# Performance work log

Hardware: AMD Instinct MI355X
Metric: run time of the kernel (lower is better)

Reference implementation:

```python
import jax, jax.numpy as jnp
import numpy as np

LOAD_BALANCE_WEIGHT = 0.05


def setup_inputs() -> dict:
    key = jax.random.key(0)
    ks = jax.random.split(key, 8)
    B, H, C, E = 8192, 4096, 1000, 4
    s_h = 1.0 / np.sqrt(H)
    return {
        "x": jax.random.normal(ks[0], (B, H), dtype=jnp.float32),
        "Wr": jax.random.normal(ks[1], (H, E), dtype=jnp.float32) * s_h,
        "br": jnp.zeros((E,), dtype=jnp.float32),
        "W1": jax.random.normal(ks[2], (E, H, H), dtype=jnp.float32) * s_h,
        "b1": jnp.zeros((E, H), dtype=jnp.float32),
        "W2": jax.random.normal(ks[3], (E, H, C), dtype=jnp.float32) * s_h,
        "b2": jnp.zeros((E, C), dtype=jnp.float32),
    }


def reference(x, Wr, br, W1, b1, W2, b2):
    # Router: linear gate -> softmax probs (eval mode: no noise)
    E = Wr.shape[1]
    router_logits = x @ Wr + br                     # [B, E]
    routing_weights = jax.nn.softmax(router_logits, axis=-1)
    # Hard top-1 dispatch
    idx = jnp.argmax(routing_weights, axis=-1)      # [B]
    onehot = jax.nn.one_hot(idx, E, dtype=x.dtype)  # [B, E]
    # Switch-style load-balance loss: E * sum(fraction_e * mean_prob_e)
    frac = onehot.mean(axis=0)                      # [E]
    mean_p = routing_weights.mean(axis=0)           # [E]
    load_balance_loss = LOAD_BALANCE_WEIGHT * E * jnp.sum(frac * mean_p)
    # Dense all-expert compute, then hard-select per token (same math as
    # gather/scatter dispatch in the torch loop, fully vectorized)
    h = jax.nn.gelu(jnp.einsum('bh,ehk->ebk', x, W1) + b1[:, None, :])  # [E,B,H]
    expert_out = jnp.einsum('ebk,ekc->ebc', h, W2) + b2[:, None, :]     # [E,B,C]
    logits = jnp.einsum('be,ebc->bc', onehot, expert_out)               # [B,C]
    return logits, load_balance_loss, routing_weights
```

## Files before the change

### kernel.cpp

```cpp
#include <hip/hip_runtime.h>
#include <hip/hip_bf16.h>

#define NB 8192
#define NH 4096
#define NC 1000
#define NE 4
#define NCP 1024

typedef __attribute__((ext_vector_type(4))) float f32x4;
typedef __attribute__((ext_vector_type(8))) short s16x8;
typedef __attribute__((ext_vector_type(4))) unsigned int u32x4;

__device__ __forceinline__ unsigned cvtpk(float a, float b){
  unsigned r; asm("v_cvt_pk_bf16_f32 %0, %1, %2" : "=v"(r) : "v"(a), "v"(b)); return r;
}
__device__ __forceinline__ int swz_off(int r, int s){
  return (r << 6) + (((s ^ (r ^ (r >> 2))) & 3) << 4);
}

__device__ __forceinline__ void gload16(const void* g, void* l) {
  __builtin_amdgcn_global_load_lds(
      (const __attribute__((address_space(1))) unsigned int*)g,
      (__attribute__((address_space(3))) unsigned int*)l, 16, 0, 0);
}

__device__ __forceinline__ void transpose_body(
    const float* __restrict__ ine, __hip_bfloat16* __restrict__ oute,
    int R, int C, int r0, int c0, int t)
{
  int c = c0 + (t << 2);
  unsigned o[4][16];
  if (c < C) {
    #pragma unroll
    for (int rp = 0; rp < 16; rp++) {
      f32x4 v0 = *(const f32x4*)(ine + (size_t)(r0 + 2*rp)     * C + c);
      f32x4 v1 = *(const f32x4*)(ine + (size_t)(r0 + 2*rp + 1) * C + c);
      #pragma unroll
      for (int j = 0; j < 4; j++) o[j][rp] = cvtpk(v0[j], v1[j]);
    }
  } else {
    #pragma unroll
    for (int j = 0; j < 4; j++)
      #pragma unroll
      for (int rp = 0; rp < 16; rp++) o[j][rp] = 0;
  }
  #pragma unroll
  for (int j = 0; j < 4; j++) {
    u32x4* dst = (u32x4*)(oute + (size_t)(c + j) * R + r0);
    dst[0] = (u32x4){ o[j][0],  o[j][1],  o[j][2],  o[j][3]  };
    dst[1] = (u32x4){ o[j][4],  o[j][5],  o[j][6],  o[j][7]  };
    dst[2] = (u32x4){ o[j][8],  o[j][9],  o[j][10], o[j][11] };
    dst[3] = (u32x4){ o[j][12], o[j][13], o[j][14], o[j][15] };
  }
}

__global__ __launch_bounds__(256) void prep_k(
    const float* __restrict__ x, const float* __restrict__ Wr,
    const float* __restrict__ br, float* __restrict__ out,
    int* __restrict__ idx, int* __restrict__ cnt_part, float* __restrict__ sum_part,
    __hip_bfloat16* __restrict__ xb,
    const float* __restrict__ W1, __hip_bfloat16* __restrict__ W1t,
    const float* __restrict__ W2, __hip_bfloat16* __restrict__ W2t)
{
  int blk = blockIdx.x, t = threadIdx.x;
  if (blk < 2048) {
    int e = blk >> 9, by = (blk >> 2) & 127, bx = blk & 3;
    transpose_body(W1 + (size_t)e * NH * NH, W1t + (size_t)e * NH * NH,
                   NH, NH, by << 5, bx << 10, t);
    return;
  }
  if (blk < 2560) {
    int bb = blk - 2048;
    int e = bb >> 7, by = bb & 127;
    transpose_body(W2 + (size_t)e * NH * NC, W2t + (size_t)e * NCP * NH,
                   NH, NC, by << 5, 0, t);
    return;
  }
  int b = blk - 2560;
  const float* xr = x + (size_t)b * NH;
  int h0 = t << 4;
  f32x4 v[4];
  #pragma unroll
  for (int j = 0; j < 4; j++) v[j] = *(const f32x4*)(xr + h0 + (j << 2));
  u32x4 ob0 = { cvtpk(v[0][0],v[0][1]), cvtpk(v[0][2],v[0][3]),
                cvtpk(v[1][0],v[1][1]), cvtpk(v[1][2],v[1][3]) };
  u32x4 ob1 = { cvtpk(v[2][0],v[2][1]), cvtpk(v[2][2],v[2][3]),
                cvtpk(v[3][0],v[3][1]), cvtpk(v[3][2],v[3][3]) };
  *(u32x4*)(xb + (size_t)b * NH + h0) = ob0;
  *(u32x4*)(xb + (size_t)b * NH + h0 + 8) = ob1;

  double a0=0, a1=0, a2=0, a3=0;
  #pragma unroll
  for (int i = 0; i < 16; i++) {
    float xv = v[i >> 2][i & 3];
    f32x4 w = *(const f32x4*)(Wr + (size_t)(h0 + i) * 4);
    double xd = (double)xv;
    a0 += xd * (double)w[0]; a1 += xd * (double)w[1];
    a2 += xd * (double)w[2]; a3 += xd * (double)w[3];
  }
  for (int off = 32; off; off >>= 1) {
    a0 += __shfl_down(a0, off); a1 += __shfl_down(a1, off);
    a2 += __shfl_down(a2, off); a3 += __shfl_down(a3, off);
  }
  __shared__ double red[4][4];
  int wid = t >> 6;
  if ((t & 63) == 0) { red[wid][0]=a0; red[wid][1]=a1; red[wid][2]=a2; red[wid][3]=a3; }
  __syncthreads();
  if (t == 0) {
    double l[4];
    for (int e = 0; e < 4; e++)
      l[e] = red[0][e] + red[1][e] + red[2][e] + red[3][e] + (double)br[e];
    int am = 0; double mx = l[0];
    for (int e = 1; e < 4; e++) if (l[e] > mx) { mx = l[e]; am = e; }
    double p[4], s = 0;
    for (int e = 0; e < 4; e++) { p[e] = exp(l[e] - mx); s += p[e]; }
    float* rw = out + (size_t)NB * NC + 1 + (size_t)b * 4;
    int bin = (b & 63) * 4;
    for (int e = 0; e < 4; e++) {
      float pe = (float)(p[e] / s);
      rw[e] = pe;
      atomicAdd(&sum_part[bin + e], pe);
    }
    idx[b] = am;
    atomicAdd(&cnt_part[bin + am], 1);
  }
}

__global__ __launch_bounds__(256) void router_k(
    const float* __restrict__ x, const float* __restrict__ Wr,
    const float* __restrict__ br, float* __restrict__ out,
    int* __restrict__ idx, int* __restrict__ cnt_part, float* __restrict__ sum_part)
{
  int b = blockIdx.x, t = threadIdx.x;
  const float* xr = x + (size_t)b * NH;
  double a0=0, a1=0, a2=0, a3=0;
  for (int i = 0; i < 16; i++) {
    int h = t + (i << 8);
    float xv = xr[h];
    f32x4 w = *(const f32x4*)(Wr + (size_t)h * 4);
    double xd = (double)xv;
    a0 += xd * (double)w[0]; a1 += xd * (double)w[1];
    a2 += xd * (double)w[2]; a3 += xd * (double)w[3];
  }
  for (int off = 32; off; off >>= 1) {
    a0 += __shfl_down(a0, off); a1 += __shfl_down(a1, off);
    a2 += __shfl_down(a2, off); a3 += __shfl_down(a3, off);
  }
  __shared__ double red[4][4];
  int wid = t >> 6;
  if ((t & 63) == 0) { red[wid][0]=a0; red[wid][1]=a1; red[wid][2]=a2; red[wid][3]=a3; }
  __syncthreads();
  if (t == 0) {
    double l[4];
    for (int e = 0; e < 4; e++)
      l[e] = red[0][e] + red[1][e] + red[2][e] + red[3][e] + (double)br[e];
    int am = 0; double mx = l[0];
    for (int e = 1; e < 4; e++) if (l[e] > mx) { mx = l[e]; am = e; }
    double p[4], s = 0;
    for (int e = 0; e < 4; e++) { p[e] = exp(l[e] - mx); s += p[e]; }
    float* rw = out + (size_t)NB * NC + 1 + (size_t)b * 4;
    int bin = (b & 63) * 4;
    for (int e = 0; e < 4; e++) {
      float pe = (float)(p[e] / s);
      rw[e] = pe;
      atomicAdd(&sum_part[bin + e], pe);
    }
    idx[b] = am;
    atomicAdd(&cnt_part[bin + am], 1);
  }
}

__global__ void finalize_k(const int* __restrict__ cnt_part, const float* __restrict__ sum_part,
                           int* __restrict__ counts, int* __restrict__ offs, float* __restrict__ out)
{
  int t = threadIdx.x;
  __shared__ int cc[4]; __shared__ float ss[4];
  if (t < 4) {
    int c = 0; float s = 0;
    for (int i = 0; i < 64; i++) { c += cnt_part[i*4 + t]; s += sum_part[i*4 + t]; }
    cc[t] = c; ss[t] = s; counts[t] = c;
  }
  __syncthreads();
  if (t == 0) {
    int o = 0; float loss = 0.f;
    for (int e = 0; e < 4; e++) {
      offs[e] = o; o += cc[e];
      loss += ((float)cc[e] / (float)NB) * (ss[e] / (float)NB);
    }
    out[(size_t)NB * NC] = 0.05f * (float)NE * loss;
  }
}

__global__ __launch_bounds__(256) void scatter_k(
    const int* __restrict__ idx, const int* __restrict__ offs,
    int* __restrict__ cursors, int* __restrict__ perm)
{
  int b = blockIdx.x * 256 + threadIdx.x;
  int e = idx[b];
  int lane = threadIdx.x & 63;
  for (int e2 = 0; e2 < 4; e2++) {
    unsigned long long m = __ballot(e == e2);
    if (e == e2) {
      int nbelow = __popcll(m & ((1ULL << lane) - 1ULL));
      int base = 0;
      if (nbelow == 0) base = atomicAdd(&cursors[e2], (int)__popcll(m));
      int src = __ffsll((long long)m) - 1;
      base = __shfl(base, src);
      perm[offs[e2] + base + nbelow] = b;
    }
  }
}

__global__ __launch_bounds__(256) void transpose_k(
    const float* __restrict__ in, __hip_bfloat16* __restrict__ outp,
    int R, int C, int Cout)
{
  int e = blockIdx.z;
  transpose_body(in + (size_t)e * R * C, outp + (size_t)e * Cout * R,
                 R, C, blockIdx.y << 5, blockIdx.x << 10, threadIdx.x);
}


#define DSR(off) (*(const s16x8*)(lds + (off)))

template<int MODE>
__global__ __launch_bounds__(256, 4) void gemmsb_k(
    const __hip_bfloat16* __restrict__ Ax, const __hip_bfloat16* __restrict__ Bw,
    const float* __restrict__ bias, const int* __restrict__ perm,
    const int* __restrict__ counts, const int* __restrict__ offs,
    __hip_bfloat16* __restrict__ H1out, float* __restrict__ out)
{
  int e = blockIdx.z;
  int cnt = counts[e];
  if (cnt == 0) return;

  const int NX = (MODE == 0 ? 32 : 8);
  const int NWG = NX * 64;
  const int CPX = NWG / 8;
  int flat = blockIdx.x + NX * blockIdx.y;
  int lg = (flat & 7) * CPX + (flat >> 3);
  int by = lg & 63;
  int bx = lg >> 6;

  int m0 = by << 7;
  if (m0 >= cnt) return;
  int seg = offs[e];
  int n0 = bx << 7;
  const __hip_bfloat16* Be = Bw + (size_t)e * (size_t)(MODE == 0 ? NH : NCP) * NH;

  __shared__ __align__(16) char lds[32768];
  __shared__ int rowtok[128];

  int tid = threadIdx.x;
  if (tid < 128) {
    int rr = m0 + tid; if (rr >= cnt) rr = cnt - 1;
    rowtok[tid] = perm[seg + rr];
  }
  __syncthreads();

  int lane = tid & 63, w = tid >> 6;
  int wr = w >> 1, wc = w & 1;
  int cx = lane & 15, g = lane >> 4;
  int l8 = lane >> 3, l7 = lane & 7;

  int srcoff = (l7 ^ l8) << 3;
  const __hip_bfloat16* pA[4];
  const __hip_bfloat16* pB[4];
  #pragma unroll
  for (int i = 0; i < 4; i++) {
    int r = w * 32 + i * 8 + l8;
    if constexpr (MODE == 0) {
      pA[i] = Ax + (size_t)rowtok[r] * NH + srcoff;
    } else {
      int rr = m0 + r; if (rr >= cnt) rr = cnt - 1;
      pA[i] = Ax + (size_t)(seg + rr) * NH + srcoff;
    }
    pB[i] = Be + (size_t)(n0 + r) * NH + srcoff;
  }
  int wst = w * 4096;

  int swz0 = ((0 * 4 + g) ^ (cx & 7)) << 4;
  int swz1 = ((1 * 4 + g) ^ (cx & 7)) << 4;
  int arow = (wr * 64 + cx) * 128;
  int brow = (wc * 64 + cx) * 128;

  f32x4 acc[4][4] = {};

  const int NT = NH / 64;

  for (int t = 0; t < NT; t++) {
    gload16(pA[0] + (size_t)t*64, lds + wst);
    gload16(pA[1] + (size_t)t*64, lds + wst + 1024);
    gload16(pA[2] + (size_t)t*64, lds + wst + 2048);
    gload16(pA[3] + (size_t)t*64, lds + wst + 3072);
    gload16(pB[0] + (size_t)t*64, lds + 16384 + wst);
    gload16(pB[1] + (size_t)t*64, lds + 16384 + wst + 1024);
    gload16(pB[2] + (size_t)t*64, lds + 16384 + wst + 2048);
    gload16(pB[3] + (size_t)t*64, lds + 16384 + wst + 3072);
    __syncthreads();

    s16x8 a0_[4], b0_[4], a1_[4], b1_[4];
    #pragma unroll
    for (int mf = 0; mf < 4; mf++) a0_[mf] = DSR(arow + mf*2048 + swz0);
    #pragma unroll
    for (int nf = 0; nf < 4; nf++) b0_[nf] = DSR(16384 + brow + nf*2048 + swz0);
    #pragma unroll
    for (int mf = 0; mf < 4; mf++)
      #pragma unroll
      for (int nf = 0; nf < 4; nf++)
        acc[mf][nf] = __builtin_amdgcn_mfma_f32_16x16x32_bf16(a0_[mf], b0_[nf], acc[mf][nf], 0, 0, 0);
    #pragma unroll
    for (int mf = 0; mf < 4; mf++) a1_[mf] = DSR(arow + mf*2048 + swz1);
    #pragma unroll
    for (int nf = 0; nf < 4; nf++) b1_[nf] = DSR(16384 + brow + nf*2048 + swz1);
    #pragma unroll
    for (int mf = 0; mf < 4; mf++)
      #pragma unroll
      for (int nf = 0; nf < 4; nf++)
        acc[mf][nf] = __builtin_amdgcn_mfma_f32_16x16x32_bf16(a1_[mf], b1_[nf], acc[mf][nf], 0, 0, 0);
    __syncthreads();
  }

  #pragma unroll
  for (int nf = 0; nf < 4; nf++) {
    int n = n0 + wc * 64 + nf * 16 + cx;
    if (MODE == 0 || n < NC) {
      float bv = bias[(size_t)e * (MODE == 0 ? NH : NC) + n];
      #pragma unroll
      for (int mf = 0; mf < 4; mf++) {
        f32x4 vacc = acc[mf][nf];
        #pragma unroll
        for (int i = 0; i < 4; i++) {
          int mrow = wr * 64 + mf * 16 + g * 4 + i;
          int mseg = m0 + mrow;
          if (mseg < cnt) {
            float u = vacc[i] + bv;
            if constexpr (MODE == 0) {
              float th = tanhf(0.79788456080286535588f * (u + 0.044715f * u * u * u));
              float hv = 0.5f * u * (1.0f + th);
              H1out[(size_t)(seg + mseg) * NH + n] = __float2bfloat16(hv);
            } else {
              int tok = rowtok[mrow];
              out[(size_t)tok * NC + n] = u;
            }
          }
        }
      }
    }
  }
}

__global__ __launch_bounds__(256) void gemm1_k(
    const float* __restrict__ x, const float* __restrict__ W1,
    const float* __restrict__ b1, const int* __restrict__ perm,
    const int* __restrict__ counts, const int* __restrict__ offs,
    __hip_bfloat16* __restrict__ H1)
{
  int e = blockIdx.z;
  int cnt = counts[e];
  int m0 = blockIdx.y << 7;
  if (m0 >= cnt) return;
  int seg = offs[e];
  int n0 = blockIdx.x << 7;
  const float* W1e = W1 + (size_t)e * NH * NH;

  __shared__ __align__(16) char As[128*32*2];
  __shared__ __align__(16) char Bs[128*32*2];
  __shared__ int rowtok[128];

  int t = threadIdx.x;
  if (t < 128) {
    int rr = m0 + t; if (rr >= cnt) rr = cnt - 1;
    rowtok[t] = perm[seg + rr];
  }
  __syncthreads();

  int ar0 = t >> 2, as_ = t & 3;
  int ar1 = ar0 + 64;
  const float* asrc0 = x + (size_t)rowtok[ar0] * NH + (as_ << 3);
  const float* asrc1 = x + (size_t)rowtok[ar1] * NH + (as_ << 3);
  int aw0 = swz_off(ar0, as_), aw1 = swz_off(ar1, as_);
  int bnc = t & 31, bkp = t >> 5;
  const float* bsrc0 = W1e + (size_t)(bkp << 1) * NH + n0 + (bnc << 2);
  const float* bsrc1 = bsrc0 + (size_t)16 * NH;

  f32x4 acc[4][4] = {};

  int lane = t & 63, wid = t >> 6;
  int wm = (wid >> 1) << 6, wn = (wid & 1) << 6;
  int g = lane >> 4, cx = lane & 15;
  int aoff[4], boff[4];
  #pragma unroll
  for (int f = 0; f < 4; f++) {
    aoff[f] = swz_off(wm + (f << 4) + cx, g);
    boff[f] = swz_off(wn + (f << 4) + cx, g);
  }

  for (int kt = 0; kt < NH; kt += 32) {
    {
      f32x4 v0 = *(const f32x4*)(asrc0 + kt);
      f32x4 v1 = *(const f32x4*)(asrc0 + kt + 4);
      u32x4 wv = { cvtpk(v0[0],v0[1]), cvtpk(v0[2],v0[3]), cvtpk(v1[0],v1[1]), cvtpk(v1[2],v1[3]) };
      *(u32x4*)(As + aw0) = wv;
      f32x4 u0 = *(const f32x4*)(asrc1 + kt);
      f32x4 u1 = *(const f32x4*)(asrc1 + kt + 4);
      u32x4 w2 = { cvtpk(u0[0],u0[1]), cvtpk(u0[2],u0[3]), cvtpk(u1[0],u1[1]), cvtpk(u1[2],u1[3]) };
      *(u32x4*)(As + aw1) = w2;
    }
    {
      const float* p0 = bsrc0 + (size_t)kt * NH;
      f32x4 rr0 = *(const f32x4*)p0;
      f32x4 rr1 = *(const f32x4*)(p0 + NH);
      int kp = bkp, sl = kp >> 2, sub = (kp & 3) << 2;
      #pragma unroll
      for (int j = 0; j < 4; j++) {
        int n = (bnc << 2) + j;
        *(unsigned*)(Bs + (n << 6) + (((sl ^ (n ^ (n >> 2))) & 3) << 4) + sub) = cvtpk(rr0[j], rr1[j]);
      }
      const float* p1 = bsrc1 + (size_t)kt * NH;
      f32x4 q0 = *(const f32x4*)p1;
      f32x4 q1 = *(const f32x4*)(p1 + NH);
      kp = bkp + 8; sl = kp >> 2; sub = (kp & 3) << 2;
      #pragma unroll
      for (int j = 0; j < 4; j++) {
        int n = (bnc << 2) + j;
        *(unsigned*)(Bs + (n << 6) + (((sl ^ (n ^ (n >> 2))) & 3) << 4) + sub) = cvtpk(q0[j], q1[j]);
      }
    }
    __syncthreads();
    s16x8 af[4], bfr[4];
    #pragma unroll
    for (int f = 0; f < 4; f++) {
      af[f]  = *(const s16x8*)(As + aoff[f]);
      bfr[f] = *(const s16x8*)(Bs + boff[f]);
    }
    #pragma unroll
    for (int mf = 0; mf < 4; mf++)
      #pragma unroll
      for (int nf = 0; nf < 4; nf++)
        acc[mf][nf] = __builtin_amdgcn_mfma_f32_16x16x32_bf16(af[mf], bfr[nf], acc[mf][nf], 0, 0, 0);
    __syncthreads();
  }

  const float* b1e = b1 + (size_t)e * NH;
  #pragma unroll
  for (int nf = 0; nf < 4; nf++) {
    int n = n0 + wn + (nf << 4) + cx;
    float bv = b1e[n];
    #pragma unroll
    for (int mf = 0; mf < 4; mf++) {
      #pragma unroll
      for (int i = 0; i < 4; i++) {
        int mseg = m0 + wm + (mf << 4) + (g << 2) + i;
        if (mseg < cnt) {
          float u = acc[mf][nf][i] + bv;
          float th = tanhf(0.79788456080286535588f * (u + 0.044715f * u * u * u));
          float hv = 0.5f * u * (1.0f + th);
          H1[(size_t)(seg + mseg) * NH + n] = __float2bfloat16(hv);
        }
      }
    }
  }
}

__global__ __launch_bounds__(256) void gemm2_k(
    const __hip_bfloat16* __restrict__ H1, const float* __restrict__ W2,
    const float* __restrict__ b2, const int* __restrict__ perm,
    const int* __restrict__ counts, const int* __restrict__ offs,
    float* __restrict__ out)
{
  int e = blockIdx.z;
  int cnt = counts[e];
  int m0 = blockIdx.y << 7;
  if (m0 >= cnt) return;
  int seg = offs[e];
  int n0 = blockIdx.x << 7;
  const float* W2e = W2 + (size_t)e * NH * NC;

  __shared__ __align__(16) char As[128*32*2];
  __shared__ __align__(16) char Bs[128*32*2];
  __shared__ int rowtok[128];

  int t = threadIdx.x;
  if (t < 128) {
    int rr = m0 + t; if (rr >= cnt) rr = cnt - 1;
    rowtok[t] = perm[seg + rr];
  }
  __syncthreads();

  int ar0 = t >> 2, as_ = t & 3;
  int ar1 = ar0 + 64;
  int rA0 = m0 + ar0; if (rA0 >= cnt) rA0 = cnt - 1;
  int rA1 = m0 + ar1; if (rA1 >= cnt) rA1 = cnt - 1;
  const __hip_bfloat16* asrc0 = H1 + (size_t)(seg + rA0) * NH + (as_ << 3);
  const __hip_bfloat16* asrc1 = H1 + (size_t)(seg + rA1) * NH + (as_ << 3);
  int aw0 = swz_off(ar0, as_), aw1 = swz_off(ar1, as_);

  int bnc = t & 31, bkp = t >> 5;
  int col = n0 + (bnc << 2);
  bool bvalid = col < NC;
  const float* bsrc0 = W2e + (size_t)(bkp << 1) * NC + col;
  const float* bsrc1 = bsrc0 + (size_t)16 * NC;

  f32x4 acc[4][4] = {};

  int lane = t & 63, wid = t >> 6;
  int wm = (wid >> 1) << 6, wn = (wid & 1) << 6;
  int g = lane >> 4, cx = lane & 15;
  int aoff[4], boff[4];
  #pragma unroll
  for (int f = 0; f < 4; f++) {
    aoff[f] = swz_off(wm + (f << 4) + cx, g);
    boff[f] = swz_off(wn + (f << 4) + cx, g);
  }

  for (int kt = 0; kt < NH; kt += 32) {
    {
      *(u32x4*)(As + aw0) = *(const u32x4*)(asrc0 + kt);
      *(u32x4*)(As + aw1) = *(const u32x4*)(asrc1 + kt);
    }
    {
      f32x4 rr0 = {}, rr1 = {}, q0 = {}, q1 = {};
      if (bvalid) {
        const float* p0 = bsrc0 + (size_t)kt * NC;
        rr0 = *(const f32x4*)p0; rr1 = *(const f32x4*)(p0 + NC);
        const float* p1 = bsrc1 + (size_t)kt * NC;
        q0 = *(const f32x4*)p1; q1 = *(const f32x4*)(p1 + NC);
      }
      int kp = bkp, sl = kp >> 2, sub = (kp & 3) << 2;
      #pragma unroll
      for (int j = 0; j < 4; j++) {
        int n = (bnc << 2) + j;
        *(unsigned*)(Bs + (n << 6) + (((sl ^ (n ^ (n >> 2))) & 3) << 4) + sub) = cvtpk(rr0[j], rr1[j]);
      }
      kp = bkp + 8; sl = kp >> 2; sub = (kp & 3) << 2;
      #pragma unroll
      for (int j = 0; j < 4; j++) {
        int n = (bnc << 2) + j;
        *(unsigned*)(Bs + (n << 6) + (((sl ^ (n ^ (n >> 2))) & 3) << 4) + sub) = cvtpk(q0[j], q1[j]);
      }
    }
    __syncthreads();
    s16x8 af[4], bfr[4];
    #pragma unroll
    for (int f = 0; f < 4; f++) {
      af[f]  = *(const s16x8*)(As + aoff[f]);
      bfr[f] = *(const s16x8*)(Bs + boff[f]);
    }
    #pragma unroll
    for (int mf = 0; mf < 4; mf++)
      #pragma unroll
      for (int nf = 0; nf < 4; nf++)
        acc[mf][nf] = __builtin_amdgcn_mfma_f32_16x16x32_bf16(af[mf], bfr[nf], acc[mf][nf], 0, 0, 0);
    __syncthreads();
  }

  const float* b2e = b2 + (size_t)e * NC;
  #pragma unroll
  for (int nf = 0; nf < 4; nf++) {
    int n = n0 + wn + (nf << 4) + cx;
    if (n < NC) {
      float bv = b2e[n];
      #pragma unroll
      for (int mf = 0; mf < 4; mf++) {
        #pragma unroll
        for (int i = 0; i < 4; i++) {
          int mseg = m0 + wm + (mf << 4) + (g << 2) + i;
          if (mseg < cnt) {
            int tok = rowtok[wm + (mf << 4) + (g << 2) + i];
            out[(size_t)tok * NC + n] = acc[mf][nf][i] + bv;
          }
        }
      }
    }
  }
}

extern "C" void kernel_launch(void* const* d_in, const int* in_sizes, int n_in,
                              void* d_out, int out_size, void* d_ws, size_t ws_size,
                              hipStream_t stream) {
  const float* x  = (const float*)d_in[0];
  const float* Wr = (const float*)d_in[1];
  const float* br = (const float*)d_in[2];
  const float* W1 = (const float*)d_in[3];
  const float* b1 = (const float*)d_in[4];
  const float* W2 = (const float*)d_in[5];
  const float* b2 = (const float*)d_in[6];
  float* out = (float*)d_out;

  char* ws = (char*)d_ws;
  const size_t SZ_XB  = (size_t)NB * NH * 2;
  const size_t SZ_H1  = (size_t)NB * NH * 2;
  const size_t SZ_W1T = (size_t)NE * NH * NH * 2;
  const size_t SZ_W2T = (size_t)NE * NCP * NH * 2;
  const size_t need = SZ_XB + SZ_H1 + SZ_W1T + SZ_W2T + (size_t)NB*4*2 + 4096;

  if (ws_size >= need) {
    size_t o = 0;
    __hip_bfloat16* xb  = (__hip_bfloat16*)(ws + o); o += SZ_XB;
    __hip_bfloat16* H1  = (__hip_bfloat16*)(ws + o); o += SZ_H1;
    __hip_bfloat16* W1t = (__hip_bfloat16*)(ws + o); o += SZ_W1T;
    __hip_bfloat16* W2t = (__hip_bfloat16*)(ws + o); o += SZ_W2T;
    int* idx  = (int*)(ws + o); o += (size_t)NB * 4;
    int* perm = (int*)(ws + o); o += (size_t)NB * 4;
    char* small = ws + o;
    int*   cursors  = (int*)(small);
    int*   counts   = (int*)(small + 16);
    int*   offs     = (int*)(small + 32);
    int*   cnt_part = (int*)(small + 64);
    float* sum_part = (float*)(small + 64 + 1024);

    hipMemsetAsync(small, 0, 64 + 2048, stream);
    prep_k<<<10752, 256, 0, stream>>>(x, Wr, br, out, idx, cnt_part, sum_part, xb,
                                      W1, W1t, W2, W2t);
    finalize_k<<<1, 64, 0, stream>>>(cnt_part, sum_part, counts, offs, out);
    scatter_k<<<NB / 256, 256, 0, stream>>>(idx, offs, cursors, perm);
    gemmsb_k<0><<<dim3(32, 64, 4), 256, 0, stream>>>(xb, W1t, b1, perm, counts, offs, H1, nullptr);
    gemmsb_k<1><<<dim3(8, 64, 4), 256, 0, stream>>>(H1, W2t, b2, perm, counts, offs, nullptr, out);
  } else {
    __hip_bfloat16* H1 = (__hip_bfloat16*)ws;
    size_t o = (size_t)NB * NH * 2;
    int* idx  = (int*)(ws + o); o += (size_t)NB * 4;
    int* perm = (int*)(ws + o); o += (size_t)NB * 4;
    char* small = ws + o;
    int*   cursors  = (int*)(small);
    int*   counts   = (int*)(small + 16);
    int*   offs     = (int*)(small + 32);
    int*   cnt_part = (int*)(small + 64);
    float* sum_part = (float*)(small + 64 + 1024);

    hipMemsetAsync(small, 0, 64 + 2048, stream);
    router_k<<<NB, 256, 0, stream>>>(x, Wr, br, out, idx, cnt_part, sum_part);
    finalize_k<<<1, 64, 0, stream>>>(cnt_part, sum_part, counts, offs, out);
    scatter_k<<<NB / 256, 256, 0, stream>>>(idx, offs, cursors, perm);
    gemm1_k<<<dim3(32, 64, 4), 256, 0, stream>>>(x, W1, b1, perm, counts, offs, H1);
    gemm2_k<<<dim3(8, 64, 4), 256, 0, stream>>>(H1, W2, b2, perm, counts, offs, out);
  }
}
```

Before: 750.6 us.

## Add 256x256-tile 8-wave GEMM1 kernel with double-buffered LDS pipeline

Replaces the 128x128-tile first expert GEMM with a new 512-thread kernel computing 256x256 output tiles, using 128KB of double-buffered LDS. Global-to-LDS loads are interleaved with MFMA phases, and it uses explicit vmcnt waits, barriers and setprio. Larger tiles raise arithmetic intensity and cut redundant global traffic for W1 and the gathered activations. The cost is lower occupancy and more tail waste on partially filled expert row blocks. It also removes the XCD-aware block remapping in gemmsb_k and lowers its launch-bounds occupancy hint.

```diff
diff --git a/kernel.cpp b/kernel.cpp
--- a/kernel.cpp
+++ b/kernel.cpp
@@ -221,10 +221,155 @@
 }
 
 
+#define DSR8(off) (*(const s16x8*)(lds + (off)))
+#define VMW4 asm volatile("s_waitcnt vmcnt(4)" ::: "memory")
+#define VMW0 asm volatile("s_waitcnt vmcnt(0)" ::: "memory")
+#define NOWAIT do{}while(0)
+#define NOSTG  do{}while(0)
+
+#define STG_A(TT,H) do{ \
+  gload16(pA[H][0] + (size_t)(TT)*64, lds + ((TT)&1)*32768 + (H)*16384 + wbase); \
+  gload16(pA[H][1] + (size_t)(TT)*64, lds + ((TT)&1)*32768 + (H)*16384 + wbase + 1024); \
+}while(0)
+#define STG_B(TT,H) do{ \
+  gload16(pB[H][0] + (size_t)(TT)*64, lds + 65536 + ((TT)&1)*32768 + (H)*16384 + wbase); \
+  gload16(pB[H][1] + (size_t)(TT)*64, lds + 65536 + ((TT)&1)*32768 + (H)*16384 + wbase + 1024); \
+}while(0)
+
+#define PH8(BB, MH, NQ, STG, WT) do{ \
+  s16x8 a_[4][2], b_[2][2]; \
+  _Pragma("unroll") \
+  for (int mf = 0; mf < 4; mf++) { \
+    a_[mf][0] = DSR8((BB)*32768 + (MH)*16384 + arow + mf*2048 + swz0); \
+    a_[mf][1] = DSR8((BB)*32768 + (MH)*16384 + arow + mf*2048 + swz1); \
+  } \
+  _Pragma("unroll") \
+  for (int nf = 0; nf < 2; nf++) { \
+    b_[nf][0] = DSR8(65536 + (BB)*32768 + (NQ)*16384 + brow + nf*2048 + swz0); \
+    b_[nf][1] = DSR8(65536 + (BB)*32768 + (NQ)*16384 + brow + nf*2048 + swz1); \
+  } \
+  STG; \
+  WT; \
+  __builtin_amdgcn_s_barrier(); \
+  __builtin_amdgcn_s_setprio(1); \
+  _Pragma("unroll") \
+  for (int mf = 0; mf < 4; mf++) \
+    _Pragma("unroll") \
+    for (int nf = 0; nf < 2; nf++) { \
+      acc[(MH)*2+(NQ)][mf][nf] = __builtin_amdgcn_mfma_f32_16x16x32_bf16(a_[mf][0], b_[nf][0], acc[(MH)*2+(NQ)][mf][nf], 0, 0, 0); \
+      acc[(MH)*2+(NQ)][mf][nf] = __builtin_amdgcn_mfma_f32_16x16x32_bf16(a_[mf][1], b_[nf][1], acc[(MH)*2+(NQ)][mf][nf], 0, 0, 0); \
+    } \
+  __builtin_amdgcn_s_setprio(0); \
+  __builtin_amdgcn_s_barrier(); \
+}while(0)
+
+__global__ __launch_bounds__(512, 2) void gemm1v2_k(
+    const __hip_bfloat16* __restrict__ Ax, const __hip_bfloat16* __restrict__ Bw,
+    const float* __restrict__ bias, const int* __restrict__ perm,
+    const int* __restrict__ counts, const int* __restrict__ offs,
+    __hip_bfloat16* __restrict__ H1out)
+{
+  int e = blockIdx.z;
+  int cnt = counts[e];
+  if (cnt == 0) return;
+  int m0 = blockIdx.y << 8;
+  if (m0 >= cnt) return;
+  int seg = offs[e];
+  int n0 = blockIdx.x << 8;
+  const __hip_bfloat16* Be = Bw + (size_t)e * NH * NH;
+
+  __shared__ __align__(16) char lds[131072];
+  __shared__ int rowtok[256];
+
+  int tid = threadIdx.x;
+  if (tid < 256) {
+    int rr = m0 + tid; if (rr >= cnt) rr = cnt - 1;
+    rowtok[tid] = perm[seg + rr];
+  }
+  __syncthreads();
+
+  int lane = tid & 63, w = tid >> 6;
+  int wr = w >> 2, wc = w & 3;
+  int cx = lane & 15, g = lane >> 4;
+  int l8 = lane >> 3, l7 = lane & 7;
+
+  int srcoff = (l7 ^ l8) << 3;
+  const __hip_bfloat16* pA[2][2];
+  const __hip_bfloat16* pB[2][2];
+  #pragma unroll
+  for (int h = 0; h < 2; h++)
+    #pragma unroll
+    for (int p = 0; p < 2; p++) {
+      int r = h * 128 + w * 16 + p * 8 + l8;
+      pA[h][p] = Ax + (size_t)rowtok[r] * NH + srcoff;
+      pB[h][p] = Be + (size_t)(n0 + r) * NH + srcoff;
+    }
+  int wbase = w * 2048;
+
+  int swz0 = ((0 * 4 + g) ^ (cx & 7)) << 4;
+  int swz1 = ((1 * 4 + g) ^ (cx & 7)) << 4;
+  int arow = (wr * 64 + cx) * 128;
+  int brow = (wc * 32 + cx) * 128;
+
+  f32x4 acc[4][4][2] = {};
+
+  const int NT = NH / 64;
+
+  STG_A(0,0); STG_B(0,0); STG_B(0,1); STG_A(0,1); STG_A(1,0); STG_B(1,0);
+  VMW4;
+  __builtin_amdgcn_s_barrier();
+
+  #pragma unroll 1
+  for (int tt = 0; tt <= NT - 4; tt += 2) {
+    PH8(0, 0, 0, STG_B(tt+1,1), NOWAIT);
+    PH8(0, 0, 1, STG_A(tt+1,1), NOWAIT);
+    PH8(0, 1, 0, STG_A(tt+2,0), NOWAIT);
+    PH8(0, 1, 1, STG_B(tt+2,0), VMW4);
+    PH8(1, 0, 0, STG_B(tt+2,1), NOWAIT);
+    PH8(1, 0, 1, STG_A(tt+2,1), NOWAIT);
+    PH8(1, 1, 0, STG_A(tt+3,0), NOWAIT);
+    PH8(1, 1, 1, STG_B(tt+3,0), VMW4);
+  }
+  PH8(0, 0, 0, STG_B(NT-1,1), NOWAIT);
+  PH8(0, 0, 1, STG_A(NT-1,1), NOWAIT);
+  PH8(0, 1, 0, NOSTG, NOWAIT);
+  PH8(0, 1, 1, NOSTG, VMW0);
+  PH8(1, 0, 0, NOSTG, NOWAIT);
+  PH8(1, 0, 1, NOSTG, NOWAIT);
+  PH8(1, 1, 0, NOSTG, NOWAIT);
+  PH8(1, 1, 1, NOSTG, NOWAIT);
+
+  const float* be_ = bias + (size_t)e * NH;
+  #pragma unroll
+  for (int mh = 0; mh < 2; mh++)
+  #pragma unroll
+  for (int nq = 0; nq < 2; nq++)
+  #pragma unroll
+  for (int nf = 0; nf < 2; nf++) {
+    int n = n0 + nq * 128 + wc * 32 + nf * 16 + cx;
+    float bv = be_[n];
+    #pragma unroll
+    for (int mf = 0; mf < 4; mf++) {
+      f32x4 vacc = acc[mh*2+nq][mf][nf];
+      #pragma unroll
+      for (int i = 0; i < 4; i++) {
+        int mrow = mh * 128 + wr * 64 + mf * 16 + g * 4 + i;
+        int mseg = m0 + mrow;
+        if (mseg < cnt) {
+          float u = vacc[i] + bv;
+          float th = tanhf(0.79788456080286535588f * (u + 0.044715f * u * u * u));
+          float hv = 0.5f * u * (1.0f + th);
+          H1out[(size_t)(seg + mseg) * NH + n] = __float2bfloat16(hv);
+        }
+      }
+    }
+  }
+}
+
 #define DSR(off) (*(const s16x8*)(lds + (off)))
 
 template<int MODE>
-__global__ __launch_bounds__(256, 4) void gemmsb_k(
+__global__ __launch_bounds__(256, 3) void gemmsb_k(
     const __hip_bfloat16* __restrict__ Ax, const __hip_bfloat16* __restrict__ Bw,
     const float* __restrict__ bias, const int* __restrict__ perm,
     const int* __restrict__ counts, const int* __restrict__ offs,
@@ -233,19 +378,10 @@
   int e = blockIdx.z;
   int cnt = counts[e];
   if (cnt == 0) return;
-
-  const int NX = (MODE == 0 ? 32 : 8);
-  const int NWG = NX * 64;
-  const int CPX = NWG / 8;
-  int flat = blockIdx.x + NX * blockIdx.y;
-  int lg = (flat & 7) * CPX + (flat >> 3);
-  int by = lg & 63;
-  int bx = lg >> 6;
-
-  int m0 = by << 7;
+  int m0 = blockIdx.y << 7;
   if (m0 >= cnt) return;
   int seg = offs[e];
-  int n0 = bx << 7;
+  int n0 = blockIdx.x << 7;
   const __hip_bfloat16* Be = Bw + (size_t)e * (size_t)(MODE == 0 ? NH : NCP) * NH;
 
   __shared__ __align__(16) char lds[32768];
@@ -615,7 +751,7 @@
                                       W1, W1t, W2, W2t);
     finalize_k<<<1, 64, 0, stream>>>(cnt_part, sum_part, counts, offs, out);
     scatter_k<<<NB / 256, 256, 0, stream>>>(idx, offs, cursors, perm);
-    gemmsb_k<0><<<dim3(32, 64, 4), 256, 0, stream>>>(xb, W1t, b1, perm, counts, offs, H1, nullptr);
+    gemm1v2_k<<<dim3(16, 32, 4), 512, 0, stream>>>(xb, W1t, b1, perm, counts, offs, H1);
     gemmsb_k<1><<<dim3(8, 64, 4), 256, 0, stream>>>(H1, W2t, b2, perm, counts, offs, nullptr, out);
   } else {
     __hip_bfloat16* H1 = (__hip_bfloat16*)ws;
```

Measured after the change: 914.9 us. 21.9% more time.
